# Performance work log

Hardware: AMD Instinct MI355X
Metric: run time of the kernel (lower is better)

Reference implementation:

```python
import jax, jax.numpy as jnp
import numpy as np

N_NODES = 100000
N_EDGES = 3200000
N_GRAPHS = 64
IN_DIM = 64
LATENT = 64
DIST_STD = 1.0


def _gcn_conv(x, W, b, src, dst, dinv):
    """PyG GCNConv: out = D^-1/2 (A+I) D^-1/2 (x W) + b, with dinv = deg^-1/2."""
    n = x.shape[0]
    h = x @ W  # [N, out]
    coef = dinv[src] * dinv[dst]  # per-edge norm
    agg = jax.ops.segment_sum(h[src] * coef[:, None], dst, num_segments=n)
    # self-loop contribution with norm dinv[i]^2
    return agg + h * (dinv * dinv)[:, None] + b


def _mean_pool(x, batch, num_graphs):
    sums = jax.ops.segment_sum(x, batch, num_segments=num_graphs)
    cnts = jax.ops.segment_sum(jnp.ones((x.shape[0],), x.dtype), batch, num_segments=num_graphs)
    return sums / jnp.maximum(cnts, 1.0)[:, None]


def setup_inputs() -> dict:
    key = jax.random.key(0)
    ks = jax.random.split(key, 12)
    x = jax.random.normal(ks[0], (N_NODES, IN_DIM), jnp.float32)
    edge_index = jax.random.randint(ks[1], (2, N_EDGES), 0, N_NODES, jnp.int64 if jax.config.jax_enable_x64 else jnp.int32).astype(jnp.int32)
    batch = jnp.sort(jax.random.randint(ks[2], (N_NODES,), 0, N_GRAPHS)).astype(jnp.int32)

    def glorot(k, shape):
        fan_in, fan_out = shape
        s = jnp.sqrt(6.0 / (fan_in + fan_out))
        return jax.random.uniform(k, shape, jnp.float32, -s, s)

    return {
        "x": x, "edge_index": edge_index, "batch": batch,
        "W1m": glorot(ks[3], (IN_DIM, 16)), "b1m": jnp.zeros((16,), jnp.float32),
        "W2m": glorot(ks[4], (16, 32)), "b2m": jnp.zeros((32,), jnp.float32),
        "W3m": glorot(ks[5], (32, LATENT)), "b3m": jnp.zeros((LATENT,), jnp.float32),
        "W1l": glorot(ks[6], (IN_DIM, 16)), "b1l": jnp.zeros((16,), jnp.float32),
        "W2l": glorot(ks[7], (16, 32)), "b2l": jnp.zeros((32,), jnp.float32),
        "W3l": glorot(ks[8], (32, LATENT)), "b3l": jnp.zeros((LATENT,), jnp.float32),
        "Wfc": glorot(ks[9], (LATENT, 160000)), "bfc": jnp.zeros((160000,), jnp.float32),
        "eps": jax.random.normal(ks[10], (N_GRAPHS, LATENT), jnp.float32) * DIST_STD,
    }


def reference(x, edge_index, batch, W1m, b1m, W2m, b2m, W3m, b3m,
              W1l, b1l, W2l, b2l, W3l, b3l, Wfc, bfc, eps):
    src, dst = edge_index[0], edge_index[1]
    n = x.shape[0]
    # degrees include self-loop (+1)
    deg = jax.ops.segment_sum(jnp.ones((src.shape[0],), x.dtype), dst, num_segments=n) + 1.0
    dinv = jax.lax.rsqrt(deg)

    mu = jax.nn.relu(_gcn_conv(x, W1m, b1m, src, dst, dinv))
    mu = jax.nn.relu(_gcn_conv(mu, W2m, b2m, src, dst, dinv))
    mu = jax.nn.relu(_gcn_conv(mu, W3m, b3m, src, dst, dinv))
    mu = _mean_pool(mu, batch, N_GRAPHS)

    log = jax.nn.relu(_gcn_conv(x, W1l, b1l, src, dst, dinv))
    log = jax.nn.relu(_gcn_conv(log, W2l, b2l, src, dst, dinv))
    log = jax.nn.relu(_gcn_conv(log, W3l, b3l, src, dst, dinv))
    logvar = _mean_pool(log, batch, N_GRAPHS)

    # latent sample (training mode): z = mu + eps * exp(0.5*logvar)
    z = mu + eps * jnp.exp(0.5 * logvar)

    # decode: sigmoid(z Wfc + bfc) -> [G, 400, 400]
    output = jax.nn.sigmoid(z @ Wfc + bfc).reshape(-1, 400, 400)
    return output, mu, logvar
```

## Files before the change

### kernel.cpp

```cpp
#include <hip/hip_runtime.h>
#include <hip/hip_bf16.h>

#define N_NODES 100000
#define N_EDGES 3200000
#define N_GRAPHS 64
#define NB 391
#define KCH 8192
#define NCHUNK ((N_EDGES + KCH - 1) / KCH)
#define MAXBKT 10240

__device__ __forceinline__ void atomAddF(float* p, float v) {
    unsafeAtomicAdd(p, v);
}

__device__ __forceinline__ float lo2f(unsigned u) { return __uint_as_float(u << 16); }
__device__ __forceinline__ float hi2f(unsigned u) { return __uint_as_float(u & 0xFFFF0000u); }
__device__ __forceinline__ unsigned pack2(float a, float b) {
    unsigned ha = __bfloat16_as_ushort(__float2bfloat16(a));
    unsigned hb = __bfloat16_as_ushort(__float2bfloat16(b));
    return ha | (hb << 16);
}

__global__ __launch_bounds__(512) void k_binCount(const int* __restrict__ dst,
                                                  int* __restrict__ gcount) {
    __shared__ int hist[NB];
    for (int t = threadIdx.x; t < NB; t += 512) hist[t] = 0;
    __syncthreads();
    int base = blockIdx.x * KCH;
    int cnt = min(KCH, N_EDGES - base);
    for (int i = threadIdx.x; i < cnt; i += 512)
        atomicAdd(&hist[dst[base + i] >> 8], 1);
    __syncthreads();
    for (int t = threadIdx.x; t < NB; t += 512)
        if (hist[t]) atomicAdd(&gcount[t], hist[t]);
}

__global__ __launch_bounds__(512) void k_scanB(const int* __restrict__ gcount,
                                               int* __restrict__ gbase,
                                               int* __restrict__ gcursor,
                                               int* __restrict__ rowptr) {
    __shared__ int s[512];
    int v = (threadIdx.x < NB) ? gcount[threadIdx.x] : 0;
    s[threadIdx.x] = v;
    __syncthreads();
    for (int off = 1; off < 512; off <<= 1) {
        int t = (threadIdx.x >= off) ? s[threadIdx.x - off] : 0;
        __syncthreads();
        s[threadIdx.x] += t;
        __syncthreads();
    }
    if (threadIdx.x < NB) {
        int e = s[threadIdx.x] - v;
        gbase[threadIdx.x] = e;
        gcursor[threadIdx.x] = e;
    }
    if (threadIdx.x == 0) rowptr[N_NODES] = N_EDGES;
}

__global__ __launch_bounds__(512) void k_binA(const int* __restrict__ src,
                                              const int* __restrict__ dst,
                                              int* __restrict__ gcursor,
                                              int* __restrict__ binned) {
    __shared__ int hist[512];
    __shared__ int sc[512];
    __shared__ int sexc[512];
    __shared__ int rbase[512];
    __shared__ int stage[KCH];
    hist[threadIdx.x] = 0;
    __syncthreads();
    int base = blockIdx.x * KCH;
    int cnt = min(KCH, N_EDGES - base);
    int myb[16], mypos[16];
    int nmine = 0;
    for (int i = 0; i < 16; ++i) {
        int idx = i * 512 + threadIdx.x;
        if (idx < cnt) {
            int b = dst[base + idx] >> 8;
            myb[nmine] = b;
            mypos[nmine] = atomicAdd(&hist[b], 1);
            ++nmine;
        }
    }
    __syncthreads();
    int v = hist[threadIdx.x];
    sc[threadIdx.x] = v;
    __syncthreads();
    for (int off = 1; off < 512; off <<= 1) {
        int t = (threadIdx.x >= off) ? sc[threadIdx.x - off] : 0;
        __syncthreads();
        sc[threadIdx.x] += t;
        __syncthreads();
    }
    sexc[threadIdx.x] = sc[threadIdx.x] - v;
    __syncthreads();
    if (threadIdx.x < NB && v > 0)
        rbase[threadIdx.x] = atomicAdd(&gcursor[threadIdx.x], v);
    for (int k = 0; k < nmine; ++k) {
        int e = base + k * 512 + threadIdx.x;
        int p = ((dst[e] & 255) << 24) | src[e];
        stage[sexc[myb[k]] + mypos[k]] = p;
    }
    __syncthreads();
    for (int j = threadIdx.x; j < cnt; j += 512) {
        int lo = 0, hi = NB - 1;
        while (lo < hi) {
            int mid = (lo + hi + 1) >> 1;
            if (sexc[mid] <= j) lo = mid; else hi = mid - 1;
        }
        binned[rbase[lo] + (j - sexc[lo])] = stage[j];
    }
}

__global__ __launch_bounds__(512) void k_passB(const int* __restrict__ gbase,
                                               int* __restrict__ csr,
                                               int* __restrict__ rowptr,
                                               float* __restrict__ dinv) {
    int b = blockIdx.x;
    int rb = gbase[b];
    int re = (b == NB - 1) ? N_EDGES : gbase[b + 1];
    int cnt = re - rb;
    int nbase = b << 8;
    int nn = min(nbase + 256, N_NODES) - nbase;
    __shared__ int stage[MAXBKT];
    __shared__ int nhist[256];
    __shared__ int sc[256];
    __shared__ int ncur[256];
    for (int t = threadIdx.x; t < 256; t += 512) nhist[t] = 0;
    __syncthreads();
    for (int j = threadIdx.x; j < cnt; j += 512) {
        int p = csr[rb + j];
        stage[j] = p;
        atomicAdd(&nhist[((unsigned)p) >> 24], 1);
    }
    __syncthreads();
    if (threadIdx.x < 256) sc[threadIdx.x] = nhist[threadIdx.x];
    __syncthreads();
    for (int off = 1; off < 256; off <<= 1) {
        int t = (threadIdx.x < 256 && threadIdx.x >= off) ? sc[threadIdx.x - off] : 0;
        __syncthreads();
        if (threadIdx.x < 256) sc[threadIdx.x] += t;
        __syncthreads();
    }
    if (threadIdx.x < 256) {
        int e = sc[threadIdx.x] - nhist[threadIdx.x];
        ncur[threadIdx.x] = e;
        if (threadIdx.x < nn) {
            rowptr[nbase + threadIdx.x] = rb + e;
            dinv[nbase + threadIdx.x] = rsqrtf((float)nhist[threadIdx.x] + 1.0f);
        }
    }
    __syncthreads();
    for (int j = threadIdx.x; j < cnt; j += 512) {
        int p = stage[j];
        int slot = atomicAdd(&ncur[((unsigned)p) >> 24], 1);
        csr[rb + slot] = p;
    }
}

template<int LOGW, bool BIAS_RELU, bool OB, bool PRE>
__global__ void __launch_bounds__(256) k_gatherB(
        const int* __restrict__ rowptr, const int* __restrict__ csr,
        const unsigned* __restrict__ in ,
        const float* __restrict__ dinv,
        const float* __restrict__ ba, const float* __restrict__ bb,
        void* __restrict__ out) {
    constexpr int W8 = (1 << LOGW) / 8;
    constexpr int NPB = 256 / W8;
    int n = blockIdx.x * NPB + (threadIdx.x / W8);
    if (n >= N_NODES) return;
    int sub = threadIdx.x % W8;
    const uint4* in4 = (const uint4*)in;
    uint4 u = in4[(size_t)n * W8 + sub];
    float a0 = lo2f(u.x), a1 = hi2f(u.x), a2 = lo2f(u.y), a3 = hi2f(u.y);
    float a4 = lo2f(u.z), a5 = hi2f(u.z), a6 = lo2f(u.w), a7 = hi2f(u.w);
    int j = rowptr[n], end = rowptr[n + 1];
    for (; j + 8 <= end; j += 8) {
        int s0 = csr[j] & 0xFFFFFF;
        int s1 = csr[j + 1] & 0xFFFFFF;
        int s2 = csr[j + 2] & 0xFFFFFF;
        int s3 = csr[j + 3] & 0xFFFFFF;
        int s4 = csr[j + 4] & 0xFFFFFF;
        int s5 = csr[j + 5] & 0xFFFFFF;
        int s6 = csr[j + 6] & 0xFFFFFF;
        int s7 = csr[j + 7] & 0xFFFFFF;
        uint4 v0 = in4[(size_t)s0 * W8 + sub];
        uint4 v1 = in4[(size_t)s1 * W8 + sub];
        uint4 v2 = in4[(size_t)s2 * W8 + sub];
        uint4 v3 = in4[(size_t)s3 * W8 + sub];
        uint4 v4 = in4[(size_t)s4 * W8 + sub];
        uint4 v5 = in4[(size_t)s5 * W8 + sub];
        uint4 v6 = in4[(size_t)s6 * W8 + sub];
        uint4 v7 = in4[(size_t)s7 * W8 + sub];
        a0 += ((lo2f(v0.x) + lo2f(v1.x)) + (lo2f(v2.x) + lo2f(v3.x)))
            + ((lo2f(v4.x) + lo2f(v5.x)) + (lo2f(v6.x) + lo2f(v7.x)));
        a1 += ((hi2f(v0.x) + hi2f(v1.x)) + (hi2f(v2.x) + hi2f(v3.x)))
            + ((hi2f(v4.x) + hi2f(v5.x)) + (hi2f(v6.x) + hi2f(v7.x)));
        a2 += ((lo2f(v0.y) + lo2f(v1.y)) + (lo2f(v2.y) + lo2f(v3.y)))
            + ((lo2f(v4.y) + lo2f(v5.y)) + (lo2f(v6.y) + lo2f(v7.y)));
        a3 += ((hi2f(v0.y) + hi2f(v1.y)) + (hi2f(v2.y) + hi2f(v3.y)))
            + ((hi2f(v4.y) + hi2f(v5.y)) + (hi2f(v6.y) + hi2f(v7.y)));
        a4 += ((lo2f(v0.z) + lo2f(v1.z)) + (lo2f(v2.z) + lo2f(v3.z)))
            + ((lo2f(v4.z) + lo2f(v5.z)) + (lo2f(v6.z) + lo2f(v7.z)));
        a5 += ((hi2f(v0.z) + hi2f(v1.z)) + (hi2f(v2.z) + hi2f(v3.z)))
            + ((hi2f(v4.z) + hi2f(v5.z)) + (hi2f(v6.z) + hi2f(v7.z)));
        a6 += ((lo2f(v0.w) + lo2f(v1.w)) + (lo2f(v2.w) + lo2f(v3.w)))
            + ((lo2f(v4.w) + lo2f(v5.w)) + (lo2f(v6.w) + lo2f(v7.w)));
        a7 += ((hi2f(v0.w) + hi2f(v1.w)) + (hi2f(v2.w) + hi2f(v3.w)))
            + ((hi2f(v4.w) + hi2f(v5.w)) + (hi2f(v6.w) + hi2f(v7.w)));
    }
    for (; j < end; ++j) {
        int s = csr[j] & 0xFFFFFF;
        uint4 v = in4[(size_t)s * W8 + sub];
        a0 += lo2f(v.x); a1 += hi2f(v.x);
        a2 += lo2f(v.y); a3 += hi2f(v.y);
        a4 += lo2f(v.z); a5 += hi2f(v.z);
        a6 += lo2f(v.w); a7 += hi2f(v.w);
    }
    float di = dinv[n];
    a0 *= di; a1 *= di; a2 *= di; a3 *= di;
    a4 *= di; a5 *= di; a6 *= di; a7 *= di;
    if (BIAS_RELU) {
        constexpr int H = (1 << LOGW) / 2;
        int d = sub * 8;
        const float* bp = (d < H) ? (ba + d) : (bb + d - H);
        a0 = fmaxf(a0 + bp[0], 0.0f);
        a1 = fmaxf(a1 + bp[1], 0.0f);
        a2 = fmaxf(a2 + bp[2], 0.0f);
        a3 = fmaxf(a3 + bp[3], 0.0f);
        a4 = fmaxf(a4 + bp[4], 0.0f);
        a5 = fmaxf(a5 + bp[5], 0.0f);
        a6 = fmaxf(a6 + bp[6], 0.0f);
        a7 = fmaxf(a7 + bp[7], 0.0f);
    }
    if (PRE) {
        a0 *= di; a1 *= di; a2 *= di; a3 *= di;
        a4 *= di; a5 *= di; a6 *= di; a7 *= di;
    }
    if (OB) {
        ((uint4*)out)[(size_t)n * W8 + sub] =
            make_uint4(pack2(a0, a1), pack2(a2, a3), pack2(a4, a5), pack2(a6, a7));
    } else {
        constexpr int OUT4 = (1 << LOGW) / 4;
        float4* o4 = (float4*)out;
        o4[(size_t)n * OUT4 + sub * 2]     = make_float4(a0, a1, a2, a3);
        o4[(size_t)n * OUT4 + sub * 2 + 1] = make_float4(a4, a5, a6, a7);
    }
}

template<int IN_W, int OUT_HALF, int A_OFF, int A_W, int B_OFF, bool BR, bool OB, bool DS>
__global__ void k_dense4(const float* __restrict__ in,
                         const float* __restrict__ Wa, const float* __restrict__ ba,
                         const float* __restrict__ Wb, const float* __restrict__ bb,
                         const float* __restrict__ dinv,
                         void* __restrict__ out) {
    __shared__ float sWa[A_W * OUT_HALF];
    __shared__ float sWb[A_W * OUT_HALF];
    __shared__ float sba[OUT_HALF];
    __shared__ float sbb[OUT_HALF];
    for (int t = threadIdx.x; t < A_W * OUT_HALF; t += 256) {
        sWa[t] = Wa[t];
        sWb[t] = Wb[t];
    }
    if (BR && threadIdx.x < OUT_HALF) {
        sba[threadIdx.x] = ba[threadIdx.x];
        sbb[threadIdx.x] = bb[threadIdx.x];
    }
    __syncthreads();
    constexpr int TPN = OUT_HALF / 2;
    int idx = blockIdx.x * 256 + threadIdx.x;
    int n = idx / TPN;
    int q = idx % TPN;
    bool isB = (q * 4) >= OUT_HALF;
    int dd = q * 4 - (isB ? OUT_HALF : 0);
    const float* sW = isB ? sWb : sWa;
    int ko = isB ? B_OFF : A_OFF;
    float4 acc;
    if (BR) {
        const float* bp = isB ? (sbb + dd) : (sba + dd);
        acc = make_float4(bp[0], bp[1], bp[2], bp[3]);
    } else {
        acc = make_float4(0.f, 0.f, 0.f, 0.f);
    }
    const float* row = in + (size_t)n * IN_W + ko;
    #pragma unroll
    for (int k = 0; k < A_W; ++k) {
        float r = row[k];
        float4 wv = *(const float4*)&sW[k * OUT_HALF + dd];
        acc.x = fmaf(r, wv.x, acc.x);
        acc.y = fmaf(r, wv.y, acc.y);
        acc.z = fmaf(r, wv.z, acc.z);
        acc.w = fmaf(r, wv.w, acc.w);
    }
    if (BR) {
        acc.x = fmaxf(acc.x, 0.f); acc.y = fmaxf(acc.y, 0.f);
        acc.z = fmaxf(acc.z, 0.f); acc.w = fmaxf(acc.w, 0.f);
    }
    if (DS) {
        float dn = dinv[n];
        acc.x *= dn; acc.y *= dn; acc.z *= dn; acc.w *= dn;
    }
    if (OB) {
        ((uint2*)out)[idx] = make_uint2(pack2(acc.x, acc.y), pack2(acc.z, acc.w));
    } else {
        ((float4*)out)[idx] = acc;
    }
}

__global__ void k_pool2(const float* __restrict__ h3, const int* __restrict__ batch,
                        float* __restrict__ pool, int* __restrict__ cnt) {
    int g = blockIdx.x >> 2;
    int q = blockIdx.x & 3;
    __shared__ int sb[2];
    if (threadIdx.x < 2) {
        int target = g + threadIdx.x;
        int lo = 0, hi = N_NODES;
        while (lo < hi) {
            int mid = (lo + hi) >> 1;
            if (batch[mid] < target) lo = mid + 1; else hi = mid;
        }
        sb[threadIdx.x] = lo;
    }
    __syncthreads();
    int start = sb[0], end = sb[1];
    int d = threadIdx.x & 127;
    int half = threadIdx.x >> 7;
    float acc = 0.0f;
    for (int n = start + q * 2 + half; n < end; n += 8)
        acc += h3[(size_t)n * 128 + d];
    __shared__ float sred[256];
    sred[threadIdx.x] = acc;
    __syncthreads();
    if (half == 0)
        atomAddF(&pool[g * 128 + d], sred[threadIdx.x] + sred[threadIdx.x + 128]);
    if (threadIdx.x == 0 && q == 0) cnt[g] = end - start;
}

__global__ void k_final(const float* __restrict__ pool, const int* __restrict__ cnt,
                        const float* __restrict__ eps, float* __restrict__ zbuf,
                        float* __restrict__ out_mu, float* __restrict__ out_lv) {
    int idx = blockIdx.x * 256 + threadIdx.x;
    int g = idx >> 6;
    float c = fmaxf((float)cnt[g], 1.0f);
    float mu = pool[g * 128 + (idx & 63)] / c;
    float lv = pool[g * 128 + 64 + (idx & 63)] / c;
    zbuf[idx] = mu + eps[idx] * __expf(0.5f * lv);
    out_mu[idx] = mu;
    out_lv[idx] = lv;
}

__global__ void __launch_bounds__(256) k_decode(const float* __restrict__ zbuf,
                                                const float* __restrict__ Wfc,
                                                const float* __restrict__ bfc,
                                                float* __restrict__ out) {
    __shared__ float sz[64 * 64];
    for (int t = threadIdx.x; t < 4096; t += 256) sz[t] = zbuf[t];
    __syncthreads();
    int j = blockIdx.x * 256 + threadIdx.x;
    float bias = bfc[j];
    float acc[64];
    #pragma unroll
    for (int g = 0; g < 64; ++g) acc[g] = bias;
    #pragma unroll 4
    for (int k4 = 0; k4 < 16; ++k4) {
        float w0 = Wfc[(k4 * 4 + 0) * 160000 + j];
        float w1 = Wfc[(k4 * 4 + 1) * 160000 + j];
        float w2 = Wfc[(k4 * 4 + 2) * 160000 + j];
        float w3 = Wfc[(k4 * 4 + 3) * 160000 + j];
        #pragma unroll
        for (int g = 0; g < 64; ++g) {
            float4 zv = *(const float4*)&sz[g * 64 + k4 * 4];
            acc[g] = fmaf(zv.x, w0, acc[g]);
            acc[g] = fmaf(zv.y, w1, acc[g]);
            acc[g] = fmaf(zv.z, w2, acc[g]);
            acc[g] = fmaf(zv.w, w3, acc[g]);
        }
    }
    #pragma unroll
    for (int g = 0; g < 64; ++g) {
        float s = 1.0f / (1.0f + __expf(-acc[g]));
        out[g * 160000 + j] = s;
    }
}

extern "C" void kernel_launch(void* const* d_in, const int* in_sizes, int n_in,
                              void* d_out, int out_size, void* d_ws, size_t ws_size,
                              hipStream_t stream) {
    const float* x     = (const float*)d_in[0];
    const int*   ei    = (const int*)d_in[1];
    const int*   batch = (const int*)d_in[2];
    const float *W1m = (const float*)d_in[3],  *b1m = (const float*)d_in[4];
    const float *W2m = (const float*)d_in[5],  *b2m = (const float*)d_in[6];
    const float *W3m = (const float*)d_in[7],  *b3m = (const float*)d_in[8];
    const float *W1l = (const float*)d_in[9],  *b1l = (const float*)d_in[10];
    const float *W2l = (const float*)d_in[11], *b2l = (const float*)d_in[12];
    const float *W3l = (const float*)d_in[13], *b3l = (const float*)d_in[14];
    const float *Wfc = (const float*)d_in[15], *bfc = (const float*)d_in[16];
    const float *eps = (const float*)d_in[17];

    const int* srcv = ei;
    const int* dstv = ei + N_EDGES;

    char* w = (char*)d_ws;
    auto alloc = [&](size_t bytes) -> char* {
        char* p = w;
        w += (bytes + 255) & ~(size_t)255;
        return p;
    };
    int*   gcount = (int*)  alloc((size_t)NB * 4);
    int*   gbase  = (int*)  alloc((size_t)NB * 4);
    int*   gcursor= (int*)  alloc((size_t)NB * 4);
    int*   rowptr = (int*)  alloc((size_t)(N_NODES + 1) * 4);
    float* dinv   = (float*)alloc((size_t)N_NODES * 4);
    float* pool   = (float*)alloc((size_t)N_GRAPHS * 128 * 4);
    int*   cnt    = (int*)  alloc((size_t)N_GRAPHS * 4);
    float* zbuf   = (float*)alloc((size_t)N_GRAPHS * 64 * 4);
    float* arena = (float*)alloc((size_t)N_NODES * 192 * 4);
    float* A   = arena;
    float* B   = arena + (size_t)N_NODES * 64;
    int*   csr = (int*)(arena + (size_t)N_NODES * 128);
    float* h3  = B;

    float* out    = (float*)d_out;
    float* out_mu = out + 10240000;
    float* out_lv = out + 10240000 + 4096;

    hipMemsetAsync(gcount, 0, (size_t)NB * 4, stream);
    hipMemsetAsync(pool, 0, (size_t)N_GRAPHS * 128 * 4, stream);

    k_binCount<<<NCHUNK, 512, 0, stream>>>(dstv, gcount);
    k_scanB<<<1, 512, 0, stream>>>(gcount, gbase, gcursor, rowptr);
    k_binA<<<NCHUNK, 512, 0, stream>>>(srcv, dstv, gcursor, csr);
    k_passB<<<NB, 512, 0, stream>>>(gbase, csr, rowptr, dinv);

    k_dense4<64, 16, 0, 64, 0, false, true, true><<<N_NODES * 8 / 256, 256, 0, stream>>>(
        x, W1m, b1m, W1l, b1l, dinv, A);
    k_gatherB<5, true, true, true><<<(N_NODES + 63) / 64, 256, 0, stream>>>(
        rowptr, csr, (const unsigned*)A, dinv, b1m, b1l, B);

    k_gatherB<5, false, false, false><<<(N_NODES + 63) / 64, 256, 0, stream>>>(
        rowptr, csr, (const unsigned*)B, dinv, b1m, b1l, A);
    k_dense4<32, 32, 0, 16, 16, true, true, true><<<N_NODES * 16 / 256, 256, 0, stream>>>(
        A, W2m, b2m, W2l, b2l, dinv, B);

    k_gatherB<6, false, false, false><<<(N_NODES + 31) / 32, 256, 0, stream>>>(
        rowptr, csr, (const unsigned*)B, dinv, b1m, b1l, A);
    k_dense4<64, 64, 0, 32, 32, true, false, false><<<N_NODES * 32 / 256, 256, 0, stream>>>(
        A, W3m, b3m, W3l, b3l, dinv, h3);

    k_pool2<<<N_GRAPHS * 4, 256, 0, stream>>>(h3, batch, pool, cnt);
    k_final<<<16, 256, 0, stream>>>(pool, cnt, eps, zbuf, out_mu, out_lv);

    k_decode<<<625, 256, 0, stream>>>(zbuf, Wfc, bfc, out);
}
```

Baseline: 518.9 us.

## Split decode across graph halves and read transposed z via scalar loads

The final step now writes z transposed (latent index major), so the decode kernel can read z directly from global memory with uniform scalar loads instead of staging it in shared memory. Each decode block handles 32 graphs instead of 64, which doubles the grid and halves the accumulator registers to allow more occupancy. The cost is that every Wfc column is now read twice, once per graph half, and the shared-memory load plus barrier is dropped.

```diff
diff --git a/kernel.cpp b/kernel.cpp
--- a/kernel.cpp
+++ b/kernel.cpp
@@ -340,45 +340,37 @@
                         float* __restrict__ out_mu, float* __restrict__ out_lv) {
     int idx = blockIdx.x * 256 + threadIdx.x;
     int g = idx >> 6;
+    int k = idx & 63;
     float c = fmaxf((float)cnt[g], 1.0f);
-    float mu = pool[g * 128 + (idx & 63)] / c;
-    float lv = pool[g * 128 + 64 + (idx & 63)] / c;
-    zbuf[idx] = mu + eps[idx] * __expf(0.5f * lv);
+    float mu = pool[g * 128 + k] / c;
+    float lv = pool[g * 128 + 64 + k] / c;
+    zbuf[k * 64 + g] = mu + eps[idx] * __expf(0.5f * lv);
     out_mu[idx] = mu;
     out_lv[idx] = lv;
 }
 
-__global__ void __launch_bounds__(256) k_decode(const float* __restrict__ zbuf,
+__global__ void __launch_bounds__(256) k_decode(const float* __restrict__ zT,
                                                 const float* __restrict__ Wfc,
                                                 const float* __restrict__ bfc,
                                                 float* __restrict__ out) {
-    __shared__ float sz[64 * 64];
-    for (int t = threadIdx.x; t < 4096; t += 256) sz[t] = zbuf[t];
-    __syncthreads();
-    int j = blockIdx.x * 256 + threadIdx.x;
+    int j = (blockIdx.x >> 1) * 256 + threadIdx.x;
+    int gh = (blockIdx.x & 1) * 32;
+    const float* zp = zT + gh;
     float bias = bfc[j];
-    float acc[64];
+    float acc[32];
     #pragma unroll
-    for (int g = 0; g < 64; ++g) acc[g] = bias;
-    #pragma unroll 4
-    for (int k4 = 0; k4 < 16; ++k4) {
-        float w0 = Wfc[(k4 * 4 + 0) * 160000 + j];
-        float w1 = Wfc[(k4 * 4 + 1) * 160000 + j];
-        float w2 = Wfc[(k4 * 4 + 2) * 160000 + j];
-        float w3 = Wfc[(k4 * 4 + 3) * 160000 + j];
+    for (int g = 0; g < 32; ++g) acc[g] = bias;
+    #pragma unroll 8
+    for (int k = 0; k < 64; ++k) {
+        float w = Wfc[(size_t)k * 160000 + j];
         #pragma unroll
-        for (int g = 0; g < 64; ++g) {
-            float4 zv = *(const float4*)&sz[g * 64 + k4 * 4];
-            acc[g] = fmaf(zv.x, w0, acc[g]);
-            acc[g] = fmaf(zv.y, w1, acc[g]);
-            acc[g] = fmaf(zv.z, w2, acc[g]);
-            acc[g] = fmaf(zv.w, w3, acc[g]);
-        }
+        for (int g = 0; g < 32; ++g)
+            acc[g] = fmaf(zp[k * 64 + g], w, acc[g]);
     }
     #pragma unroll
-    for (int g = 0; g < 64; ++g) {
+    for (int g = 0; g < 32; ++g) {
         float s = 1.0f / (1.0f + __expf(-acc[g]));
-        out[g * 160000 + j] = s;
+        out[(size_t)(gh + g) * 160000 + j] = s;
     }
 }
 
@@ -450,5 +442,5 @@
     k_pool2<<<N_GRAPHS * 4, 256, 0, stream>>>(h3, batch, pool, cnt);
     k_final<<<16, 256, 0, stream>>>(pool, cnt, eps, zbuf, out_mu, out_lv);
 
-    k_decode<<<625, 256, 0, stream>>>(zbuf, Wfc, bfc, out);
-}
+    k_decode<<<1250, 256, 0, stream>>>(zbuf, Wfc, bfc, out);
+}
```

Result: faster. 496.2 us (-4.4%).
